# Performance work log

Measured on AMD Instinct MI355X. Metric: run time of the kernel, lower is better.

## Reference

```python
import jax, jax.numpy as jnp
import numpy as np

NUM_EXPERTS = 8
TOPK = 2


def setup_inputs() -> dict:
    key = jax.random.key(0)
    k1, k2, k3, k4 = jax.random.split(key, 4)
    T = 16384           # num_tokens * topk
    D = 2048            # intermediate_size_per_rank
    H = 4096            # hidden_dim
    intermediate_states = jax.random.normal(k1, (T, D), dtype=jnp.float32)
    w = jax.random.normal(k2, (NUM_EXPERTS, D, H), dtype=jnp.float32) * 0.02
    topk_weight = jax.random.uniform(k3, (T,), dtype=jnp.float32)
    topk_ids = jax.random.randint(k4, (T,), 0, NUM_EXPERTS, dtype=jnp.int32)
    return {"intermediate_states": intermediate_states, "w": w,
            "topk_weight": topk_weight, "topk_ids": topk_ids}


def reference(intermediate_states, w, topk_weight, topk_ids):
    # intermediate_states: [T, D] with T = num_tokens * topk
    # w: [E, D, H]; topk_ids/topk_weight: [T]
    T, D = intermediate_states.shape
    E, _, H = w.shape
    # per-expert masked matmul loop (E is small and fixed), matching the torch loop:
    # out[mask] = x[mask] @ w[i] * weight[mask]
    out = jnp.zeros((T, H), dtype=intermediate_states.dtype)
    for i in range(E):
        m = (topk_ids == i).astype(intermediate_states.dtype)[:, None]  # [T,1]
        out = out + ((intermediate_states * m) @ w[i]) * topk_weight[:, None]
    # topk-weighted sum over the topk slots per token
    output = out.reshape(T // TOPK, TOPK, H).sum(axis=1)  # [T/topk, H]
    # world_size == 1 -> reduce_scatter_tensor is the identity
    return output
```

## Files before the change

kernel.cpp:

```cpp
#include <hip/hip_runtime.h>
#include <hip/hip_bf16.h>

#define T_TOK   16384
#define DDIM    2048
#define HDIM    4096
#define NEXP    8
#define BM      256
#define BN      256
#define NKT     64
#define NKS     32
#define NBAND   (HDIM / BN)
#define MAX_TILES 72
#define KTB     16384
#define NBLK    (MAX_TILES * NBAND)

typedef __attribute__((ext_vector_type(4))) float f32x4;
typedef __attribute__((ext_vector_type(8))) __bf16 bf16x8;

#define WS_TILE_EXPERT 16
#define WS_TILE_START  (16 + MAX_TILES)
#define WS_TILE_NROWS  (16 + 2*MAX_TILES)
#define WS_ROW_IDS     1024
#define WS_SLOT_POS    18432

#define WS_APACK_OFF   131072ULL
#define WS_APACK_SZ    ((size_t)MAX_TILES * NKT * KTB)
#define WS_WB_OFF      (WS_APACK_OFF + WS_APACK_SZ)
#define WS_WB_SZ       ((size_t)NEXP * NBAND * NKT * KTB)

#define WS2_APACK_OFF  262144ULL
#define WS2_WB_OFF     (WS2_APACK_OFF + WS_APACK_SZ)
#define WS2_Y_OFF      (WS2_WB_OFF + WS_WB_SZ)
#define WS2_Y_SZ       ((size_t)T_TOK * HDIM * 2)
#define WS2_NEED       (WS2_Y_OFF + WS2_Y_SZ)


__device__ __forceinline__ void gload16(const void* g, void* l) {
    __builtin_amdgcn_global_load_lds(
        (const __attribute__((address_space(1))) void*)g,
        (__attribute__((address_space(3))) void*)l, 16, 0, 0);
}

__global__ void routing_kernel(const int* __restrict__ topk_ids, int* __restrict__ wsi,
                               int* __restrict__ slot_pos) {
    __shared__ int cnt[NEXP];
    __shared__ int base[NEXP];
    int tid = threadIdx.x;
    if (tid < NEXP) cnt[tid] = 0;
    __syncthreads();
    for (int i = tid; i < T_TOK; i += blockDim.x)
        atomicAdd(&cnt[topk_ids[i]], 1);
    __syncthreads();
    if (tid == 0) {
        int acc = 0, nt = 0;
        for (int e = 0; e < NEXP; ++e) {
            base[e] = acc;
            int c = cnt[e];
            for (int off = 0; off < c; off += BM) {
                wsi[WS_TILE_EXPERT + nt] = e;
                wsi[WS_TILE_START + nt]  = acc + off;
                wsi[WS_TILE_NROWS + nt]  = (c - off < BM) ? (c - off) : BM;
                nt++;
            }
            acc += c;
        }
        wsi[0] = nt;
    }
    __syncthreads();
    if (tid < NEXP) cnt[tid] = base[tid];
    __syncthreads();
    for (int i = tid; i < T_TOK; i += blockDim.x) {
        int pos = atomicAdd(&cnt[topk_ids[i]], 1);
        wsi[WS_ROW_IDS + pos] = i;
        if (slot_pos) slot_pos[i] = pos;
    }
}

__global__ __launch_bounds__(256)
void pack_w_kernel(const float* __restrict__ W, unsigned char* __restrict__ wb) {
    long long u = (long long)blockIdx.x * 256 + threadIdx.x;
    int n  = (int)(u % HDIM);
    int kt = (int)((u / HDIM) % NKT);
    int e  = (int)(u / ((long long)HDIM * NKT));
    const float* src = W + ((size_t)e * DDIM + (size_t)kt * 32) * HDIM + n;
    int band = n >> 8;
    int row  = n & 255;
    unsigned char* dst = wb + (((size_t)(e * NBAND + band) * NKT + kt) * KTB) + row * 64;
    const int qsw = (row >> 1) & 3;
    #pragma unroll
    for (int q = 0; q < 4; ++q) {
        bf16x8 h;
        #pragma unroll
        for (int j = 0; j < 8; ++j)
            h[j] = (__bf16)src[(size_t)(q * 8 + j) * HDIM];
        *reinterpret_cast<bf16x8*>(dst + ((q ^ qsw) << 4)) = h;
    }
}

__global__ __launch_bounds__(256)
void pack_a_kernel(const float* __restrict__ X, const int* __restrict__ wsi,
                   unsigned char* __restrict__ apack) {
    const int tile = blockIdx.x;
    if (tile >= wsi[0]) return;
    const int kt = blockIdx.y;
    const int rstart = wsi[WS_TILE_START + tile];
    const int nrows  = wsi[WS_TILE_NROWS + tile];
    const int r = threadIdx.x;
    unsigned char* dst = apack + ((size_t)tile * NKT + kt) * KTB + r * 64;
    const int qsw = (r >> 1) & 3;
    bf16x8 v0, v1, v2, v3;
    if (r < nrows) {
        int slot = wsi[WS_ROW_IDS + rstart + r];
        const f32x4* p = reinterpret_cast<const f32x4*>(X + (size_t)slot * DDIM + kt * 32);
        f32x4 f[8];
        #pragma unroll
        for (int i = 0; i < 8; ++i) f[i] = p[i];
        #pragma unroll
        for (int j = 0; j < 4; ++j) { v0[j] = (__bf16)f[0][j]; v0[4+j] = (__bf16)f[1][j]; }
        #pragma unroll
        for (int j = 0; j < 4; ++j) { v1[j] = (__bf16)f[2][j]; v1[4+j] = (__bf16)f[3][j]; }
        #pragma unroll
        for (int j = 0; j < 4; ++j) { v2[j] = (__bf16)f[4][j]; v2[4+j] = (__bf16)f[5][j]; }
        #pragma unroll
        for (int j = 0; j < 4; ++j) { v3[j] = (__bf16)f[6][j]; v3[4+j] = (__bf16)f[7][j]; }
    } else {
        #pragma unroll
        for (int j = 0; j < 8; ++j) { v0[j]=(__bf16)0.f; v1[j]=(__bf16)0.f; v2[j]=(__bf16)0.f; v3[j]=(__bf16)0.f; }
    }
    *reinterpret_cast<bf16x8*>(dst + ((0 ^ qsw) << 4)) = v0;
    *reinterpret_cast<bf16x8*>(dst + ((1 ^ qsw) << 4)) = v1;
    *reinterpret_cast<bf16x8*>(dst + ((2 ^ qsw) << 4)) = v2;
    *reinterpret_cast<bf16x8*>(dst + ((3 ^ qsw) << 4)) = v3;
}

#define GEMM_PROLOGUE_AND_MAINLOOP                                                         \
    const int id  = blockIdx.x;                                                            \
    const int swz = (id & 7) * (NBLK / 8) + (id >> 3);                                     \
    const int tile = swz / NBAND;                                                          \
    const int band = swz % NBAND;                                                          \
    if (tile >= wsi[0]) return;                                                            \
    const int e      = wsi[WS_TILE_EXPERT + tile];                                         \
    const int rstart = wsi[WS_TILE_START + tile];                                          \
    const int nrows  = wsi[WS_TILE_NROWS + tile];                                          \
    extern __shared__ unsigned char smem[];                                                \
    const int t    = threadIdx.x;                                                          \
    const int lane = t & 63;                                                               \
    const int wid  = t >> 6;                                                               \
    const int wm   = wid >> 2;                                                             \
    const int wn   = wid & 3;                                                              \
    const int r16  = lane & 15;                                                            \
    const int c16  = lane >> 4;                                                            \
    const unsigned char* agB = apack + (size_t)tile * NKT * KTB + t * 16;                  \
    const unsigned char* bgB = wb + ((size_t)(e * NBAND + band) * NKT) * KTB + t * 16;     \
    const int ldst = wid * 1024;                                                           \
    const int qswz  = c16 ^ ((r16 >> 1) & 3);                                              \
    const int abase = (wm * 128 + r16) * 64 + (qswz << 4);                                 \
    const int bbase = (wn * 64 + r16) * 64 + (qswz << 4);                                  \
    f32x4 acc[8][4];                                                                       \
    _Pragma("unroll") for (int i = 0; i < 8; ++i)                                          \
        _Pragma("unroll") for (int j = 0; j < 4; ++j)                                      \
            acc[i][j] = (f32x4)(0.0f);                                                     \
    STAGE_A(0, 0); STAGE_B(0, 0); STAGE_A(1, 0); STAGE_B(1, 0);                            \
    asm volatile("s_waitcnt vmcnt(4)" ::: "memory");                                       \
    __builtin_amdgcn_s_barrier();                                                          \
    __builtin_amdgcn_sched_barrier(0);                                                     \
    _Pragma("unroll 1")                                                                    \
    for (int ks = 0; ks < NKS - 1; ++ks) {                                                 \
        const int cb = (ks & 1) << 16;                                                     \
        const int sb = cb ^ 65536;                                                         \
        bf16x8 afr[4], bfr[4];                                                             \
        LDA(0, 0); LDB(0);                                                                 \
        STAGE_A(2 * ks + 2, sb);                                                           \
        WAIT_LGKM_MFMA_FENCE();                                                            \
        PHASE_MFMA(0);                                                                     \
        __builtin_amdgcn_s_barrier();                                                      \
        LDA(4, 0);                                                                         \
        STAGE_B(2 * ks + 2, sb);                                                           \
        asm volatile("s_waitcnt vmcnt(4)" ::: "memory");                                   \
        WAIT_LGKM_MFMA_FENCE();                                                            \
        PHASE_MFMA(4);                                                                     \
        __builtin_amdgcn_s_barrier();                                                      \
        LDA(0, 1); LDB(1);                                                                 \
        STAGE_A(2 * ks + 3, sb);                                                           \
        WAIT_LGKM_MFMA_FENCE();                                                            \
        PHASE_MFMA(0);                                                                     \
        __builtin_amdgcn_s_barrier();                                                      \
        LDA(4, 1);                                                                         \
        STAGE_B(2 * ks + 3, sb);                                                           \
        asm volatile("s_waitcnt vmcnt(4)" ::: "memory");                                   \
        WAIT_LGKM_MFMA_FENCE();                                                            \
        PHASE_MFMA(4);                                                                     \
        __builtin_amdgcn_s_barrier();                                                      \
    }                                                                                      \
    {                                                                                      \
        const int cb = ((NKS - 1) & 1) << 16;                                              \
        bf16x8 afr[4], bfr[4];                                                             \
        LDA(0, 0); LDB(0);                                                                 \
        WAIT_LGKM_MFMA_FENCE();                                                            \
        PHASE_MFMA(0);                                                                     \
        __builtin_amdgcn_s_barrier();                                                      \
        LDA(4, 0);                                                                         \
        asm volatile("s_waitcnt vmcnt(0)" ::: "memory");                                   \
        WAIT_LGKM_MFMA_FENCE();                                                            \
        PHASE_MFMA(4);                                                                     \
        __builtin_amdgcn_s_barrier();                                                      \
        LDA(0, 1); LDB(1);                                                                 \
        WAIT_LGKM_MFMA_FENCE();                                                            \
        PHASE_MFMA(0);                                                                     \
        __builtin_amdgcn_s_barrier();                                                      \
        LDA(4, 1);                                                                         \
        asm volatile("s_waitcnt lgkmcnt(0)" ::: "memory");                                 \
        __builtin_amdgcn_sched_barrier(0);                                                 \
        PHASE_MFMA(4);                                                                     \
    }

#define STAGE_A(IMG, SB) do {                                                              \
    gload16(agB + (size_t)(IMG) * KTB,        smem + (SB) + ((IMG) & 1) * 16384 + ldst);          \
    gload16(agB + (size_t)(IMG) * KTB + 8192, smem + (SB) + ((IMG) & 1) * 16384 + 8192 + ldst);   \
} while (0)
#define STAGE_B(IMG, SB) do {                                                              \
    gload16(bgB + (size_t)(IMG) * KTB,        smem + (SB) + 32768 + ((IMG) & 1) * 16384 + ldst);        \
    gload16(bgB + (size_t)(IMG) * KTB + 8192, smem + (SB) + 32768 + ((IMG) & 1) * 16384 + 8192 + ldst); \
} while (0)
#define LDA(MB, IMG) do { _Pragma("unroll") for (int mf = 0; mf < 4; ++mf)                 \
    afr[mf] = *reinterpret_cast<const bf16x8*>(smem + cb + (IMG) * 16384 + abase + ((MB) + mf) * 1024); } while (0)
#define LDB(IMG) do { _Pragma("unroll") for (int nf = 0; nf < 4; ++nf)                     \
    bfr[nf] = *reinterpret_cast<const bf16x8*>(smem + cb + 32768 + (IMG) * 16384 + bbase + nf * 1024); } while (0)
#define PHASE_MFMA(MB) do {                                                                \
    __builtin_amdgcn_s_setprio(1);                                                         \
    _Pragma("unroll") for (int mf = 0; mf < 4; ++mf)                                       \
        _Pragma("unroll") for (int nf = 0; nf < 4; ++nf)                                   \
            acc[(MB) + mf][nf] = __builtin_amdgcn_mfma_f32_16x16x32_bf16(afr[mf], bfr[nf], acc[(MB) + mf][nf], 0, 0, 0); \
    __builtin_amdgcn_s_setprio(0);                                                         \
} while (0)
#define WAIT_LGKM_MFMA_FENCE() do {                                                        \
    __builtin_amdgcn_s_barrier();                                                          \
    asm volatile("s_waitcnt lgkmcnt(0)" ::: "memory");                                     \
    __builtin_amdgcn_sched_barrier(0);                                                     \
} while (0)

__global__ __launch_bounds__(512, 2)
void gemm_fast2(const unsigned char* __restrict__ apack,
                const unsigned char* __restrict__ wb,
                const float* __restrict__ topk_weight,
                const int* __restrict__ wsi,
                __hip_bfloat16* __restrict__ yb) {
    GEMM_PROLOGUE_AND_MAINLOOP
    const int col0 = band * BN + wn * 64 + r16;
    #pragma unroll
    for (int mf = 0; mf < 8; ++mf) {
        const int rbase = wm * 128 + mf * 16 + c16 * 4;
        #pragma unroll
        for (int i = 0; i < 4; ++i) {
            int rl = rbase + i;
            if (rl < nrows) {
                int spos = rstart + rl;
                float wt = topk_weight[wsi[WS_ROW_IDS + spos]];
                __hip_bfloat16* yr = yb + (size_t)spos * HDIM + col0;
                #pragma unroll
                for (int nf = 0; nf < 4; ++nf)
                    yr[nf * 16] = (__hip_bfloat16)(acc[mf][nf][i] * wt);
            }
        }
    }
}

__global__ __launch_bounds__(512, 2)
void gemm_fast(const unsigned char* __restrict__ apack,
               const unsigned char* __restrict__ wb,
               const float* __restrict__ topk_weight,
               const int* __restrict__ wsi,
               float* __restrict__ Out) {
    GEMM_PROLOGUE_AND_MAINLOOP
    const int col0 = band * BN + wn * 64 + r16;
    #pragma unroll
    for (int mf = 0; mf < 8; ++mf) {
        const int rbase = wm * 128 + mf * 16 + c16 * 4;
        #pragma unroll
        for (int i = 0; i < 4; ++i) {
            int rl = rbase + i;
            if (rl < nrows) {
                int slot = wsi[WS_ROW_IDS + rstart + rl];
                float wt = topk_weight[slot];
                float* orow = Out + (size_t)(slot >> 1) * HDIM + col0;
                #pragma unroll
                for (int nf = 0; nf < 4; ++nf)
                    atomicAdd(orow + nf * 16, acc[mf][nf][i] * wt);
            }
        }
    }
}

__global__ __launch_bounds__(512)
void reduce_kernel(const __hip_bfloat16* __restrict__ yb,
                   const int* __restrict__ slot_pos,
                   float* __restrict__ Out) {
    const int tk = blockIdx.x;
    const int c  = threadIdx.x;
    const int p0 = slot_pos[2 * tk];
    const int p1 = slot_pos[2 * tk + 1];
    const bf16x8 a = *reinterpret_cast<const bf16x8*>(yb + (size_t)p0 * HDIM + c * 8);
    const bf16x8 b = *reinterpret_cast<const bf16x8*>(yb + (size_t)p1 * HDIM + c * 8);
    f32x4 o0, o1;
    #pragma unroll
    for (int j = 0; j < 4; ++j) o0[j] = (float)a[j] + (float)b[j];
    #pragma unroll
    for (int j = 0; j < 4; ++j) o1[j] = (float)a[4 + j] + (float)b[4 + j];
    float* orow = Out + (size_t)tk * HDIM + c * 8;
    *reinterpret_cast<f32x4*>(orow)     = o0;
    *reinterpret_cast<f32x4*>(orow + 4) = o1;
}

extern "C" void kernel_launch(void* const* d_in, const int* in_sizes, int n_in,
                              void* d_out, int out_size, void* d_ws, size_t ws_size,
                              hipStream_t stream) {
    const float* X   = (const float*)d_in[0];
    const float* W   = (const float*)d_in[1];
    const float* wgt = (const float*)d_in[2];
    const int*   ids = (const int*)d_in[3];
    float* Out = (float*)d_out;
    int*   wsi = (int*)d_ws;

    if (ws_size >= WS2_NEED) {
        unsigned char* apack = (unsigned char*)d_ws + WS2_APACK_OFF;
        unsigned char* wb    = (unsigned char*)d_ws + WS2_WB_OFF;
        __hip_bfloat16* yb   = (__hip_bfloat16*)((unsigned char*)d_ws + WS2_Y_OFF);
        int* slot_pos        = wsi + WS_SLOT_POS;
        routing_kernel<<<1, 256, 0, stream>>>(ids, wsi, slot_pos);
        pack_w_kernel<<<(NEXP * NKT * HDIM) / 256, 256, 0, stream>>>(W, wb);
        dim3 agrid(MAX_TILES, NKT, 1);
        pack_a_kernel<<<agrid, 256, 0, stream>>>(X, wsi, apack);
        gemm_fast2<<<NBLK, 512, 131072, stream>>>(apack, wb, wgt, wsi, yb);
        reduce_kernel<<<T_TOK / 2, 512, 0, stream>>>(yb, slot_pos, Out);
    } else {
        unsigned char* apack = (unsigned char*)d_ws + WS_APACK_OFF;
        unsigned char* wb    = (unsigned char*)d_ws + WS_WB_OFF;
        hipMemsetAsync(d_out, 0, (size_t)out_size * sizeof(float), stream);
        routing_kernel<<<1, 256, 0, stream>>>(ids, wsi, nullptr);
        pack_w_kernel<<<(NEXP * NKT * HDIM) / 256, 256, 0, stream>>>(W, wb);
        dim3 agrid(MAX_TILES, NKT, 1);
        pack_a_kernel<<<agrid, 256, 0, stream>>>(X, wsi, apack);
        gemm_fast<<<NBLK, 512, 131072, stream>>>(apack, wb, wgt, wsi, Out);
    }
}
```

Measured before the change: 548.0 us.

## Switch GEMM to 32x32x16 MFMA tiles and merge pack kernels into one launch

Replaces the 16x16x32 bf16 MFMA micro-tiling with 32x32x16 MFMAs, so each wave holds 4x2 accumulators of 16 floats and issues fewer LDS fragment reads per flop. The epilogue row/column mapping is rewritten to match the 32x32 output layout. Separately, the weight and activation pack kernels are fused into one launch with a combined 1D grid to cut a launch and let the two packs overlap. The larger MFMA shape changes the LDS read pattern and swizzle usage, which could add bank conflicts or register pressure.

```diff
diff --git a/kernel.cpp b/kernel.cpp
--- a/kernel.cpp
+++ b/kernel.cpp
@@ -13,9 +13,12 @@
 #define MAX_TILES 72
 #define KTB     16384
 #define NBLK    (MAX_TILES * NBAND)
-
-typedef __attribute__((ext_vector_type(4))) float f32x4;
-typedef __attribute__((ext_vector_type(8))) __bf16 bf16x8;
+#define PW_BLOCKS 8192
+#define PA_BLOCKS (MAX_TILES * NKT)
+
+typedef __attribute__((ext_vector_type(4)))  float f32x4;
+typedef __attribute__((ext_vector_type(16))) float f32x16;
+typedef __attribute__((ext_vector_type(8)))  __bf16 bf16x8;
 
 #define WS_TILE_EXPERT 16
 #define WS_TILE_START  (16 + MAX_TILES)
@@ -77,61 +80,91 @@
 }
 
 __global__ __launch_bounds__(256)
-void pack_w_kernel(const float* __restrict__ W, unsigned char* __restrict__ wb) {
-    long long u = (long long)blockIdx.x * 256 + threadIdx.x;
-    int n  = (int)(u % HDIM);
-    int kt = (int)((u / HDIM) % NKT);
-    int e  = (int)(u / ((long long)HDIM * NKT));
-    const float* src = W + ((size_t)e * DDIM + (size_t)kt * 32) * HDIM + n;
-    int band = n >> 8;
-    int row  = n & 255;
-    unsigned char* dst = wb + (((size_t)(e * NBAND + band) * NKT + kt) * KTB) + row * 64;
-    const int qsw = (row >> 1) & 3;
-    #pragma unroll
-    for (int q = 0; q < 4; ++q) {
-        bf16x8 h;
+void pack_all_kernel(const float* __restrict__ W, const float* __restrict__ X,
+                     const int* __restrict__ wsi,
+                     unsigned char* __restrict__ wb, unsigned char* __restrict__ apack) {
+    const int bid = blockIdx.x;
+    if (bid < PW_BLOCKS) {
+        long long u = (long long)bid * 256 + threadIdx.x;
+        int n  = (int)(u % HDIM);
+        int kt = (int)((u / HDIM) % NKT);
+        int e  = (int)(u / ((long long)HDIM * NKT));
+        const float* src = W + ((size_t)e * DDIM + (size_t)kt * 32) * HDIM + n;
+        int band = n >> 8;
+        int row  = n & 255;
+        unsigned char* dst = wb + (((size_t)(e * NBAND + band) * NKT + kt) * KTB) + row * 64;
+        const int qsw = (row >> 1) & 3;
         #pragma unroll
-        for (int j = 0; j < 8; ++j)
-            h[j] = (__bf16)src[(size_t)(q * 8 + j) * HDIM];
-        *reinterpret_cast<bf16x8*>(dst + ((q ^ qsw) << 4)) = h;
-    }
-}
-
-__global__ __launch_bounds__(256)
-void pack_a_kernel(const float* __restrict__ X, const int* __restrict__ wsi,
-                   unsigned char* __restrict__ apack) {
-    const int tile = blockIdx.x;
-    if (tile >= wsi[0]) return;
-    const int kt = blockIdx.y;
-    const int rstart = wsi[WS_TILE_START + tile];
-    const int nrows  = wsi[WS_TILE_NROWS + tile];
-    const int r = threadIdx.x;
-    unsigned char* dst = apack + ((size_t)tile * NKT + kt) * KTB + r * 64;
-    const int qsw = (r >> 1) & 3;
-    bf16x8 v0, v1, v2, v3;
-    if (r < nrows) {
-        int slot = wsi[WS_ROW_IDS + rstart + r];
-        const f32x4* p = reinterpret_cast<const f32x4*>(X + (size_t)slot * DDIM + kt * 32);
-        f32x4 f[8];
-        #pragma unroll
-        for (int i = 0; i < 8; ++i) f[i] = p[i];
-        #pragma unroll
-        for (int j = 0; j < 4; ++j) { v0[j] = (__bf16)f[0][j]; v0[4+j] = (__bf16)f[1][j]; }
-        #pragma unroll
-        for (int j = 0; j < 4; ++j) { v1[j] = (__bf16)f[2][j]; v1[4+j] = (__bf16)f[3][j]; }
-        #pragma unroll
-        for (int j = 0; j < 4; ++j) { v2[j] = (__bf16)f[4][j]; v2[4+j] = (__bf16)f[5][j]; }
-        #pragma unroll
-        for (int j = 0; j < 4; ++j) { v3[j] = (__bf16)f[6][j]; v3[4+j] = (__bf16)f[7][j]; }
+        for (int q = 0; q < 4; ++q) {
+            bf16x8 h;
+            #pragma unroll
+            for (int j = 0; j < 8; ++j)
+                h[j] = (__bf16)src[(size_t)(q * 8 + j) * HDIM];
+            *reinterpret_cast<bf16x8*>(dst + ((q ^ qsw) << 4)) = h;
+        }
     } else {
-        #pragma unroll
-        for (int j = 0; j < 8; ++j) { v0[j]=(__bf16)0.f; v1[j]=(__bf16)0.f; v2[j]=(__bf16)0.f; v3[j]=(__bf16)0.f; }
-    }
-    *reinterpret_cast<bf16x8*>(dst + ((0 ^ qsw) << 4)) = v0;
-    *reinterpret_cast<bf16x8*>(dst + ((1 ^ qsw) << 4)) = v1;
-    *reinterpret_cast<bf16x8*>(dst + ((2 ^ qsw) << 4)) = v2;
-    *reinterpret_cast<bf16x8*>(dst + ((3 ^ qsw) << 4)) = v3;
-}
+        const int pa = bid - PW_BLOCKS;
+        const int tile = pa >> 6;
+        const int kt   = pa & 63;
+        if (tile >= wsi[0]) return;
+        const int rstart = wsi[WS_TILE_START + tile];
+        const int nrows  = wsi[WS_TILE_NROWS + tile];
+        const int r = threadIdx.x;
+        unsigned char* dst = apack + ((size_t)tile * NKT + kt) * KTB + r * 64;
+        const int qsw = (r >> 1) & 3;
+        bf16x8 v0, v1, v2, v3;
+        if (r < nrows) {
+            int slot = wsi[WS_ROW_IDS + rstart + r];
+            const f32x4* p = reinterpret_cast<const f32x4*>(X + (size_t)slot * DDIM + kt * 32);
+            f32x4 f[8];
+            #pragma unroll
+            for (int i = 0; i < 8; ++i) f[i] = p[i];
+            #pragma unroll
+            for (int j = 0; j < 4; ++j) { v0[j] = (__bf16)f[0][j]; v0[4+j] = (__bf16)f[1][j]; }
+            #pragma unroll
+            for (int j = 0; j < 4; ++j) { v1[j] = (__bf16)f[2][j]; v1[4+j] = (__bf16)f[3][j]; }
+            #pragma unroll
+            for (int j = 0; j < 4; ++j) { v2[j] = (__bf16)f[4][j]; v2[4+j] = (__bf16)f[5][j]; }
+            #pragma unroll
+            for (int j = 0; j < 4; ++j) { v3[j] = (__bf16)f[6][j]; v3[4+j] = (__bf16)f[7][j]; }
+        } else {
+            #pragma unroll
+            for (int j = 0; j < 8; ++j) { v0[j]=(__bf16)0.f; v1[j]=(__bf16)0.f; v2[j]=(__bf16)0.f; v3[j]=(__bf16)0.f; }
+        }
+        *reinterpret_cast<bf16x8*>(dst + ((0 ^ qsw) << 4)) = v0;
+        *reinterpret_cast<bf16x8*>(dst + ((1 ^ qsw) << 4)) = v1;
+        *reinterpret_cast<bf16x8*>(dst + ((2 ^ qsw) << 4)) = v2;
+        *reinterpret_cast<bf16x8*>(dst + ((3 ^ qsw) << 4)) = v3;
+    }
+}
+
+#define STAGE_A(IMG, SB) do {                                                              \
+    gload16(agB + (size_t)(IMG) * KTB,        smem + (SB) + ((IMG) & 1) * 16384 + ldst);          \
+    gload16(agB + (size_t)(IMG) * KTB + 8192, smem + (SB) + ((IMG) & 1) * 16384 + 8192 + ldst);   \
+} while (0)
+#define STAGE_B(IMG, SB) do {                                                              \
+    gload16(bgB + (size_t)(IMG) * KTB,        smem + (SB) + 32768 + ((IMG) & 1) * 16384 + ldst);        \
+    gload16(bgB + (size_t)(IMG) * KTB + 8192, smem + (SB) + 32768 + ((IMG) & 1) * 16384 + 8192 + ldst); \
+} while (0)
+#define LDA2(MB, IMG) do { _Pragma("unroll") for (int f = 0; f < 2; ++f) {                 \
+    afr[f][0] = *reinterpret_cast<const bf16x8*>(smem + cb + (IMG) * 16384 + arb + ((MB) + f) * 2048 + q0); \
+    afr[f][1] = *reinterpret_cast<const bf16x8*>(smem + cb + (IMG) * 16384 + arb + ((MB) + f) * 2048 + q1); } } while (0)
+#define LDB2(IMG) do { _Pragma("unroll") for (int nf = 0; nf < 2; ++nf) {                  \
+    bfr[nf][0] = *reinterpret_cast<const bf16x8*>(smem + cb + 32768 + (IMG) * 16384 + brb + nf * 2048 + q0); \
+    bfr[nf][1] = *reinterpret_cast<const bf16x8*>(smem + cb + 32768 + (IMG) * 16384 + brb + nf * 2048 + q1); } } while (0)
+#define PHASE_MFMA2(MB) do {                                                               \
+    __builtin_amdgcn_s_setprio(1);                                                         \
+    _Pragma("unroll") for (int f = 0; f < 2; ++f)                                          \
+        _Pragma("unroll") for (int nf = 0; nf < 2; ++nf)                                   \
+            _Pragma("unroll") for (int h = 0; h < 2; ++h)                                  \
+                acc[(MB) + f][nf] = __builtin_amdgcn_mfma_f32_32x32x16_bf16(afr[f][h], bfr[nf][h], acc[(MB) + f][nf], 0, 0, 0); \
+    __builtin_amdgcn_s_setprio(0);                                                         \
+} while (0)
+#define WAIT_LGKM_MFMA_FENCE() do {                                                        \
+    __builtin_amdgcn_s_barrier();                                                          \
+    asm volatile("s_waitcnt lgkmcnt(0)" ::: "memory");                                     \
+    __builtin_amdgcn_sched_barrier(0);                                                     \
+} while (0)
 
 #define GEMM_PROLOGUE_AND_MAINLOOP                                                         \
     const int id  = blockIdx.x;                                                            \
@@ -148,18 +181,20 @@
     const int wid  = t >> 6;                                                               \
     const int wm   = wid >> 2;                                                             \
     const int wn   = wid & 3;                                                              \
-    const int r16  = lane & 15;                                                            \
-    const int c16  = lane >> 4;                                                            \
+    const int l31  = lane & 31;                                                            \
+    const int lhi  = lane >> 5;                                                            \
     const unsigned char* agB = apack + (size_t)tile * NKT * KTB + t * 16;                  \
     const unsigned char* bgB = wb + ((size_t)(e * NBAND + band) * NKT) * KTB + t * 16;     \
     const int ldst = wid * 1024;                                                           \
-    const int qswz  = c16 ^ ((r16 >> 1) & 3);                                              \
-    const int abase = (wm * 128 + r16) * 64 + (qswz << 4);                                 \
-    const int bbase = (wn * 64 + r16) * 64 + (qswz << 4);                                  \
-    f32x4 acc[8][4];                                                                       \
-    _Pragma("unroll") for (int i = 0; i < 8; ++i)                                          \
-        _Pragma("unroll") for (int j = 0; j < 4; ++j)                                      \
-            acc[i][j] = (f32x4)(0.0f);                                                     \
+    const int qsw  = (l31 >> 1) & 3;                                                       \
+    const int q0   = ((0 + lhi) ^ qsw) << 4;                                               \
+    const int q1   = ((2 + lhi) ^ qsw) << 4;                                               \
+    const int arb  = (wm * 128 + l31) * 64;                                                \
+    const int brb  = (wn * 64 + l31) * 64;                                                 \
+    f32x16 acc[4][2];                                                                      \
+    _Pragma("unroll") for (int i = 0; i < 4; ++i)                                          \
+        _Pragma("unroll") for (int j = 0; j < 2; ++j)                                      \
+            acc[i][j] = (f32x16)(0.0f);                                                    \
     STAGE_A(0, 0); STAGE_B(0, 0); STAGE_A(1, 0); STAGE_B(1, 0);                            \
     asm volatile("s_waitcnt vmcnt(4)" ::: "memory");                                       \
     __builtin_amdgcn_s_barrier();                                                          \
@@ -168,76 +203,51 @@
     for (int ks = 0; ks < NKS - 1; ++ks) {                                                 \
         const int cb = (ks & 1) << 16;                                                     \
         const int sb = cb ^ 65536;                                                         \
-        bf16x8 afr[4], bfr[4];                                                             \
-        LDA(0, 0); LDB(0);                                                                 \
+        bf16x8 afr[2][2], bfr[2][2];                                                       \
+        LDA2(0, 0); LDB2(0);                                                               \
         STAGE_A(2 * ks + 2, sb);                                                           \
         WAIT_LGKM_MFMA_FENCE();                                                            \
-        PHASE_MFMA(0);                                                                     \
-        __builtin_amdgcn_s_barrier();                                                      \
-        LDA(4, 0);                                                                         \
+        PHASE_MFMA2(0);                                                                    \
+        __builtin_amdgcn_s_barrier();                                                      \
+        LDA2(2, 0);                                                                        \
         STAGE_B(2 * ks + 2, sb);                                                           \
         asm volatile("s_waitcnt vmcnt(4)" ::: "memory");                                   \
         WAIT_LGKM_MFMA_FENCE();                                                            \
-        PHASE_MFMA(4);                                                                     \
-        __builtin_amdgcn_s_barrier();                                                      \
-        LDA(0, 1); LDB(1);                                                                 \
+        PHASE_MFMA2(2);                                                                    \
+        __builtin_amdgcn_s_barrier();                                                      \
+        LDA2(0, 1); LDB2(1);                                                               \
         STAGE_A(2 * ks + 3, sb);                                                           \
         WAIT_LGKM_MFMA_FENCE();                                                            \
-        PHASE_MFMA(0);                                                                     \
-        __builtin_amdgcn_s_barrier();                                                      \
-        LDA(4, 1);                                                                         \
+        PHASE_MFMA2(0);                                                                    \
+        __builtin_amdgcn_s_barrier();                                                      \
+        LDA2(2, 1);                                                                        \
         STAGE_B(2 * ks + 3, sb);                                                           \
         asm volatile("s_waitcnt vmcnt(4)" ::: "memory");                                   \
         WAIT_LGKM_MFMA_FENCE();                                                            \
-        PHASE_MFMA(4);                                                                     \
+        PHASE_MFMA2(2);                                                                    \
         __builtin_amdgcn_s_barrier();                                                      \
     }                                                                                      \
     {                                                                                      \
         const int cb = ((NKS - 1) & 1) << 16;                                              \
-        bf16x8 afr[4], bfr[4];                                                             \
-        LDA(0, 0); LDB(0);                                                                 \
-        WAIT_LGKM_MFMA_FENCE();                                                            \
-        PHASE_MFMA(0);                                                                     \
-        __builtin_amdgcn_s_barrier();                                                      \
-        LDA(4, 0);                                                                         \
+        bf16x8 afr[2][2], bfr[2][2];                                                       \
+        LDA2(0, 0); LDB2(0);                                                               \
+        WAIT_LGKM_MFMA_FENCE();                                                            \
+        PHASE_MFMA2(0);                                                                    \
+        __builtin_amdgcn_s_barrier();                                                      \
+        LDA2(2, 0);                                                                        \
         asm volatile("s_waitcnt vmcnt(0)" ::: "memory");                                   \
         WAIT_LGKM_MFMA_FENCE();                                                            \
-        PHASE_MFMA(4);                                                                     \
-        __builtin_amdgcn_s_barrier();                                                      \
-        LDA(0, 1); LDB(1);                                                                 \
-        WAIT_LGKM_MFMA_FENCE();                                                            \
-        PHASE_MFMA(0);                                                                     \
-        __builtin_amdgcn_s_barrier();                                                      \
-        LDA(4, 1);                                                                         \
+        PHASE_MFMA2(2);                                                                    \
+        __builtin_amdgcn_s_barrier();                                                      \
+        LDA2(0, 1); LDB2(1);                                                               \
+        WAIT_LGKM_MFMA_FENCE();                                                            \
+        PHASE_MFMA2(0);                                                                    \
+        __builtin_amdgcn_s_barrier();                                                      \
+        LDA2(2, 1);                                                                        \
         asm volatile("s_waitcnt lgkmcnt(0)" ::: "memory");                                 \
         __builtin_amdgcn_sched_barrier(0);                                                 \
-        PHASE_MFMA(4);                                                                     \
-    }
-
-#define STAGE_A(IMG, SB) do {                                                              \
-    gload16(agB + (size_t)(IMG) * KTB,        smem + (SB) + ((IMG) & 1) * 16384 + ldst);          \
-    gload16(agB + (size_t)(IMG) * KTB + 8192, smem + (SB) + ((IMG) & 1) * 16384 + 8192 + ldst);   \
-} while (0)
-#define STAGE_B(IMG, SB) do {                                                              \
-    gload16(bgB + (size_t)(IMG) * KTB,        smem + (SB) + 32768 + ((IMG) & 1) * 16384 + ldst);        \
-    gload16(bgB + (size_t)(IMG) * KTB + 8192, smem + (SB) + 32768 + ((IMG) & 1) * 16384 + 8192 + ldst); \
-} while (0)
-#define LDA(MB, IMG) do { _Pragma("unroll") for (int mf = 0; mf < 4; ++mf)                 \
-    afr[mf] = *reinterpret_cast<const bf16x8*>(smem + cb + (IMG) * 16384 + abase + ((MB) + mf) * 1024); } while (0)
-#define LDB(IMG) do { _Pragma("unroll") for (int nf = 0; nf < 4; ++nf)                     \
-    bfr[nf] = *reinterpret_cast<const bf16x8*>(smem + cb + 32768 + (IMG) * 16384 + bbase + nf * 1024); } while (0)
-#define PHASE_MFMA(MB) do {                                                                \
-    __builtin_amdgcn_s_setprio(1);                                                         \
-    _Pragma("unroll") for (int mf = 0; mf < 4; ++mf)                                       \
-        _Pragma("unroll") for (int nf = 0; nf < 4; ++nf)                                   \
-            acc[(MB) + mf][nf] = __builtin_amdgcn_mfma_f32_16x16x32_bf16(afr[mf], bfr[nf], acc[(MB) + mf][nf], 0, 0, 0); \
-    __builtin_amdgcn_s_setprio(0);                                                         \
-} while (0)
-#define WAIT_LGKM_MFMA_FENCE() do {                                                        \
-    __builtin_amdgcn_s_barrier();                                                          \
-    asm volatile("s_waitcnt lgkmcnt(0)" ::: "memory");                                     \
-    __builtin_amdgcn_sched_barrier(0);                                                     \
-} while (0)
+        PHASE_MFMA2(2);                                                                    \
+    }
 
 __global__ __launch_bounds__(512, 2)
 void gemm_fast2(const unsigned char* __restrict__ apack,
@@ -246,20 +256,18 @@
                 const int* __restrict__ wsi,
                 __hip_bfloat16* __restrict__ yb) {
     GEMM_PROLOGUE_AND_MAINLOOP
-    const int col0 = band * BN + wn * 64 + r16;
+    const int col0 = band * BN + wn * 64 + l31;
     #pragma unroll
-    for (int mf = 0; mf < 8; ++mf) {
-        const int rbase = wm * 128 + mf * 16 + c16 * 4;
+    for (int mf = 0; mf < 4; ++mf) {
         #pragma unroll
-        for (int i = 0; i < 4; ++i) {
-            int rl = rbase + i;
+        for (int reg = 0; reg < 16; ++reg) {
+            const int rl = wm * 128 + mf * 32 + (reg & 3) + 8 * (reg >> 2) + 4 * lhi;
             if (rl < nrows) {
-                int spos = rstart + rl;
-                float wt = topk_weight[wsi[WS_ROW_IDS + spos]];
+                const int spos = rstart + rl;
+                const float wt = topk_weight[wsi[WS_ROW_IDS + spos]];
                 __hip_bfloat16* yr = yb + (size_t)spos * HDIM + col0;
-                #pragma unroll
-                for (int nf = 0; nf < 4; ++nf)
-                    yr[nf * 16] = (__hip_bfloat16)(acc[mf][nf][i] * wt);
+                yr[0]  = (__hip_bfloat16)(acc[mf][0][reg] * wt);
+                yr[32] = (__hip_bfloat16)(acc[mf][1][reg] * wt);
             }
         }
     }
@@ -272,20 +280,18 @@
                const int* __restrict__ wsi,
                float* __restrict__ Out) {
     GEMM_PROLOGUE_AND_MAINLOOP
-    const int col0 = band * BN + wn * 64 + r16;
+    const int col0 = band * BN + wn * 64 + l31;
     #pragma unroll
-    for (int mf = 0; mf < 8; ++mf) {
-        const int rbase = wm * 128 + mf * 16 + c16 * 4;
+    for (int mf = 0; mf < 4; ++mf) {
         #pragma unroll
-        for (int i = 0; i < 4; ++i) {
-            int rl = rbase + i;
+        for (int reg = 0; reg < 16; ++reg) {
+            const int rl = wm * 128 + mf * 32 + (reg & 3) + 8 * (reg >> 2) + 4 * lhi;
             if (rl < nrows) {
-                int slot = wsi[WS_ROW_IDS + rstart + rl];
-                float wt = topk_weight[slot];
+                const int slot = wsi[WS_ROW_IDS + rstart + rl];
+                const float wt = topk_weight[slot];
                 float* orow = Out + (size_t)(slot >> 1) * HDIM + col0;
-                #pragma unroll
-                for (int nf = 0; nf < 4; ++nf)
-                    atomicAdd(orow + nf * 16, acc[mf][nf][i] * wt);
+                atomicAdd(orow,      acc[mf][0][reg] * wt);
+                atomicAdd(orow + 32, acc[mf][1][reg] * wt);
             }
         }
     }
@@ -327,9 +333,7 @@
         __hip_bfloat16* yb   = (__hip_bfloat16*)((unsigned char*)d_ws + WS2_Y_OFF);
         int* slot_pos        = wsi + WS_SLOT_POS;
         routing_kernel<<<1, 256, 0, stream>>>(ids, wsi, slot_pos);
-        pack_w_kernel<<<(NEXP * NKT * HDIM) / 256, 256, 0, stream>>>(W, wb);
-        dim3 agrid(MAX_TILES, NKT, 1);
-        pack_a_kernel<<<agrid, 256, 0, stream>>>(X, wsi, apack);
+        pack_all_kernel<<<PW_BLOCKS + PA_BLOCKS, 256, 0, stream>>>(W, X, wsi, wb, apack);
         gemm_fast2<<<NBLK, 512, 131072, stream>>>(apack, wb, wgt, wsi, yb);
         reduce_kernel<<<T_TOK / 2, 512, 0, stream>>>(yb, slot_pos, Out);
     } else {
@@ -337,9 +341,7 @@
         unsigned char* wb    = (unsigned char*)d_ws + WS_WB_OFF;
         hipMemsetAsync(d_out, 0, (size_t)out_size * sizeof(float), stream);
         routing_kernel<<<1, 256, 0, stream>>>(ids, wsi, nullptr);
-        pack_w_kernel<<<(NEXP * NKT * HDIM) / 256, 256, 0, stream>>>(W, wb);
-        dim3 agrid(MAX_TILES, NKT, 1);
-        pack_a_kernel<<<agrid, 256, 0, stream>>>(X, wsi, apack);
+        pack_all_kernel<<<PW_BLOCKS + PA_BLOCKS, 256, 0, stream>>>(W, X, wsi, wb, apack);
         gemm_fast<<<NBLK, 512, 131072, stream>>>(apack, wb, wgt, wsi, Out);
     }
 }
```

Result: slower. 616.9 us (+12.6%).
